# Kernel optimization log

Measured on AMD Instinct MI355X. Metric: run time of the kernel, lower is better.

The kernel has to match this reference:

```python
import jax, jax.numpy as jnp
import numpy as np

B, M, IN, H, D = 64, 512, 256, 4, 64
N = B * M
E = N * 16


def setup_inputs() -> dict:
    key = jax.random.key(0)
    ks = jax.random.split(key, 12)
    s = 1.0 / np.sqrt(IN)
    return {
        "query_input": jax.random.normal(ks[0], (N, IN), jnp.float32),
        "source_input": jax.random.normal(ks[1], (N, IN), jnp.float32),
        "edge_weight": jax.random.uniform(ks[2], (E,), jnp.float32),
        "Wq_w": jax.random.normal(ks[3], (IN, H * D), jnp.float32) * s,
        "Wq_b": jax.random.normal(ks[4], (H * D,), jnp.float32) * s,
        "Wk_w": jax.random.normal(ks[5], (IN, H * D), jnp.float32) * s,
        "Wk_b": jax.random.normal(ks[6], (H * D,), jnp.float32) * s,
        "Wv_w": jax.random.normal(ks[7], (IN, H * D), jnp.float32) * s,
        "Wv_b": jax.random.normal(ks[8], (H * D,), jnp.float32) * s,
        "n_nodes": jnp.full((B,), M, jnp.int32),
        "edge_index": jax.random.randint(ks[9], (2, E), 0, N, jnp.int32),
    }


def reference(query_input, source_input, edge_weight, Wq_w, Wq_b, Wk_w, Wk_b, Wv_w, Wv_b, n_nodes, edge_index):
    # projections -> [N, H, D]
    q = (query_input @ Wq_w + Wq_b).reshape(N, H, D)
    k = (source_input @ Wk_w + Wk_b).reshape(N, H, D)
    v = (source_input @ Wv_w + Wv_b).reshape(N, H, D)

    # 'simple' kernel attention. Global L2 normalization (torch.norm over whole tensor).
    qn = q / jnp.linalg.norm(q)
    kn = k / jnp.linalg.norm(k)
    # equal-size graphs: padding + mask reduces exactly to a reshape [B, M, H, D]
    q_pad = qn.reshape(B, M, H, D)
    k_pad = kn.reshape(B, M, H, D)
    v_pad = v.reshape(B, M, H, D)
    kv = jnp.einsum('bmhk,bmhv->bhkv', k_pad, v_pad)          # per-graph K^T V
    v_sum = v_pad.sum(axis=1)                                  # [B, H, D] scatter_add over batch
    k_sum = k_pad.sum(axis=1)                                  # [B, H, D]
    numer = jnp.einsum('bmhk,bhkv->bmhv', q_pad, kv) + v_sum[:, None]
    denom = jnp.einsum('bmhk,bhk->bmh', q_pad, k_sum) + n_nodes.astype(q.dtype)[:, None, None]
    attn = (numer / denom[..., None]).reshape(N, H, D)

    # gcn_conv on value: out[c] = sum_{e: col_e = c} w_e * rsqrt(deg[col_e]*deg[row_e]) * v[row_e]
    row, col = edge_index[0], edge_index[1]
    deg = jax.ops.segment_sum(jnp.ones((E,), jnp.float32), col, num_segments=N)
    val = edge_weight / jnp.sqrt(deg[col] * deg[row])
    val = jnp.nan_to_num(val, nan=0.0, posinf=0.0, neginf=0.0)
    gcn = jax.ops.segment_sum(val[:, None, None] * v[row], col, num_segments=N)

    return (attn + gcn).mean(axis=1)  # mean over heads -> [N, D]
```

## Files before the change

kernel.cpp:

```cpp
#include <hip/hip_runtime.h>
#include <hip/hip_bf16.h>

#define NN 32768
#define BB 64
#define MM 512
#define HH 4
#define DD 64
#define INF 256
#define HD 256
#define EE 524288
#define XSZ 8388608

typedef unsigned short ushort;
typedef unsigned int uint;
typedef short s16x8 __attribute__((ext_vector_type(8)));
typedef ushort u16x8 __attribute__((ext_vector_type(8)));
typedef float f32x4 __attribute__((ext_vector_type(4)));

__device__ __forceinline__ ushort f2bf(float f) {
    uint u = __float_as_uint(f);
    return (ushort)((u + 0x7fffu + ((u >> 16) & 1u)) >> 16);
}
__device__ __forceinline__ float bf2f(ushort u) {
    return __uint_as_float((uint)u << 16);
}
__device__ __forceinline__ uint pkbf(float x, float y) {
    __hip_bfloat162 h = __float22bfloat162_rn(make_float2(x, y));
    return *(uint*)&h;
}

#define GLD16(gp, lp) __builtin_amdgcn_global_load_lds( \
    (const __attribute__((address_space(1))) void*)(gp), \
    (__attribute__((address_space(3))) void*)(lp), 16, 0, 0)

__global__ __launch_bounds__(256) void prep_kernel(
    const float* __restrict__ Wq, const float* __restrict__ Wk,
    const float* __restrict__ Wv, ushort* __restrict__ WT,
    const int* __restrict__ ei, int* __restrict__ deg,
    const float* __restrict__ Xq, const float* __restrict__ Xs,
    ushort* __restrict__ xq16, ushort* __restrict__ xs16)
{
    const int bid = blockIdx.x;
    if (bid < 768) {
        const int id = bid * 256 + threadIdx.x;
        const int mat = id >> 16, rem = id & 65535;
        const int n = rem >> 8, kk = rem & 255;
        const float* W = (mat == 0) ? Wq : (mat == 1) ? Wk : Wv;
        WT[id] = f2bf(W[kk * 256 + n]);
    } else if (bid < 2816) {
        const int e = (bid - 768) * 256 + threadIdx.x;
        atomicAdd(&deg[ei[EE + e]], 1);
    } else {
        const size_t id = (size_t)(bid - 2816) * 256 + threadIdx.x;
        const size_t o8 = id * 8;
        const float* src; ushort* dst; size_t o;
        if (o8 < XSZ) { src = Xq; dst = xq16; o = o8; }
        else          { src = Xs; dst = xs16; o = o8 - XSZ; }
        const float4 f0 = *(const float4*)(src + o);
        const float4 f1 = *(const float4*)(src + o + 4);
        u16x8 r;
        r[0] = f2bf(f0.x); r[1] = f2bf(f0.y); r[2] = f2bf(f0.z); r[3] = f2bf(f0.w);
        r[4] = f2bf(f1.x); r[5] = f2bf(f1.y); r[6] = f2bf(f1.z); r[7] = f2bf(f1.w);
        *(u16x8*)(dst + o) = r;
    }
}

__global__ __launch_bounds__(256) void qkv_scan(
    const ushort* __restrict__ Xq16, const ushort* __restrict__ Xs16,
    const ushort* __restrict__ WT,
    const float* __restrict__ bq, const float* __restrict__ bk,
    const float* __restrict__ bv,
    ushort* __restrict__ qo, ushort* __restrict__ ko, ushort* __restrict__ vo,
    float* __restrict__ sumsq,
    const int* __restrict__ deg, int* __restrict__ offsets)
{
    __shared__ ushort As[2][128 * 32];
    __shared__ ushort Bs[2][128 * 32];
    __shared__ float wred[4];
    __shared__ int part[256];

    const int id = blockIdx.x;
    const int t = threadIdx.x;

    if (id == 1536) {
        const int base = t * 128;
        int s = 0;
        for (int i = 0; i < 128; ++i) s += deg[base + i];
        part[t] = s;
        __syncthreads();
        for (int off = 1; off < 256; off <<= 1) {
            int a = part[t];
            int b2 = (t >= off) ? part[t - off] : 0;
            __syncthreads();
            part[t] = a + b2;
            __syncthreads();
        }
        int run = (t == 0) ? 0 : part[t - 1];
        for (int i = 0; i < 128; ++i) { offsets[base + i] = run; run += deg[base + i]; }
        if (t == 255) offsets[NN] = run;
        return;
    }

    const int vv = (id & 7) * 192 + (id >> 3);
    const int rt = vv / 6, ct = vv % 6;
    const int wsel = ct >> 1;
    const ushort* A16 = (wsel == 0) ? Xq16 : Xs16;
    const ushort* W   = WT + (size_t)wsel * 65536;
    const float* bias = (wsel == 0) ? bq : (wsel == 1) ? bk : bv;
    ushort* C         = (wsel == 0) ? qo : (wsel == 1) ? ko : vo;
    const int row0 = rt * 128;
    const int col0 = (ct & 1) * 128;

    const int l = t & 63, w = t >> 6;
    const int fr = l & 15, q4 = l >> 4;
    const int wr = (w & 1) * 64, wc = (w >> 1) * 64;

    const int srow = (w << 4) + (l >> 2);
    const int scol = (l & 3) << 3;
    const ushort* ga = &A16[(size_t)(row0 + srow) * INF + scol];
    const ushort* gb = &W  [(size_t)(col0 + srow) * INF + scol];
    const int lbase = (w << 9);

    f32x4 acc[4][4] = {};

    GLD16(ga,             &As[0][lbase]);
    GLD16(ga + 64 * INF,  &As[0][2048 + lbase]);
    GLD16(gb,             &Bs[0][lbase]);
    GLD16(gb + 64 * INF,  &Bs[0][2048 + lbase]);

    int cur = 0;
    for (int it = 0; it < 8; ++it) {
        __syncthreads();
        if (it < 7) {
            const int k0 = (it + 1) * 32;
            GLD16(ga + k0,            &As[cur ^ 1][lbase]);
            GLD16(ga + k0 + 64 * INF, &As[cur ^ 1][2048 + lbase]);
            GLD16(gb + k0,            &Bs[cur ^ 1][lbase]);
            GLD16(gb + k0 + 64 * INF, &Bs[cur ^ 1][2048 + lbase]);
        }
        const int kg = q4 * 8;
        s16x8 af[4], bfr[4];
#pragma unroll
        for (int i = 0; i < 4; ++i)
            af[i] = *(const s16x8*)&As[cur][(wr + i * 16 + fr) * 32 + kg];
#pragma unroll
        for (int j = 0; j < 4; ++j)
            bfr[j] = *(const s16x8*)&Bs[cur][(wc + j * 16 + fr) * 32 + kg];
#pragma unroll
        for (int i = 0; i < 4; ++i)
#pragma unroll
            for (int j = 0; j < 4; ++j)
                acc[i][j] = __builtin_amdgcn_mfma_f32_16x16x32_bf16(
                    af[i], bfr[j], acc[i][j], 0, 0, 0);
        cur ^= 1;
    }

    float loc = 0.f;
#pragma unroll
    for (int j = 0; j < 4; ++j) {
        const int colg = col0 + wc + j * 16 + fr;
        const float bj = bias[colg];
#pragma unroll
        for (int i = 0; i < 4; ++i) {
            const int rowg = row0 + wr + i * 16 + q4 * 4;
#pragma unroll
            for (int m = 0; m < 4; ++m) {
                float cv = acc[i][j][m] + bj;
                loc += cv * cv;
                C[(size_t)(rowg + m) * HD + colg] = f2bf(cv);
            }
        }
    }
    if (wsel < 2) {
#pragma unroll
        for (int off = 32; off > 0; off >>= 1) loc += __shfl_down(loc, off, 64);
        if (l == 0) wred[w] = loc;
        __syncthreads();
        if (t == 0) atomicAdd(&sumsq[wsel], wred[0] + wred[1] + wred[2] + wred[3]);
    }
}

#define KVP 136
__global__ __launch_bounds__(256) void kv_vbar(
    const ushort* __restrict__ k16, const ushort* __restrict__ v16,
    float* __restrict__ kv_p, float* __restrict__ ksum_p, float* __restrict__ vsum_p,
    float* __restrict__ vbar)
{
    __shared__ ushort kT[64 * KVP];
    __shared__ ushort vT[64 * KVP];
    const int bid = blockIdx.x;
    const int t = threadIdx.x;

    if (bid >= 1024) {
        const int idx = (bid - 1024) * 1024 + t * 4;
        const int n = idx >> 6, d0 = idx & 63;
        const ushort* vr = &v16[(size_t)n * HD + d0];
        float4 o;
        float* op = (float*)&o;
#pragma unroll
        for (int j = 0; j < 4; ++j)
            op[j] = 0.25f * (bf2f(vr[j]) + bf2f(vr[64 + j]) +
                             bf2f(vr[128 + j]) + bf2f(vr[192 + j]));
        *(float4*)&vbar[idx] = o;
        return;
    }

    const int h = bid & 3, b = (bid >> 2) & 63, z = bid >> 8;
    const int l = t & 63, w = t >> 6;
    const size_t base = (size_t)b * MM * HD + (size_t)h * DD;
    const int m0 = z * 128;

    {
        const int mat = t >> 7;
        const int u = t & 63;
        const int dhalf = (t >> 6) & 1;
        const int r0 = 2 * u;
        const int d0 = dhalf * 32;
        const ushort* src = mat ? v16 : k16;
        ushort* dst = mat ? vT : kT;
        const ushort* p0 = &src[base + (size_t)(m0 + r0) * HD + d0];
        const ushort* p1 = p0 + HD;
        u16x8 ra[4], rb[4];
#pragma unroll
        for (int i = 0; i < 4; ++i) ra[i] = *(const u16x8*)(p0 + 8 * i);
#pragma unroll
        for (int i = 0; i < 4; ++i) rb[i] = *(const u16x8*)(p1 + 8 * i);
#pragma unroll
        for (int i = 0; i < 4; ++i)
#pragma unroll
            for (int jj = 0; jj < 8; ++jj) {
                const int d = d0 + 8 * i + jj;
                uint pk = (uint)ra[i][jj] | ((uint)rb[i][jj] << 16);
                *(uint*)&dst[d * KVP + r0] = pk;
            }
    }
    __syncthreads();

    const int fr = l & 15, q4 = l >> 4, kg = q4 * 8;
    const int wr2 = (w & 1) * 32, wc2 = (w >> 1) * 32;
    s16x8 ones;
#pragma unroll
    for (int i = 0; i < 8; ++i) ones[i] = (short)0x3F80;

    f32x4 acc[2][2] = {};
    f32x4 aks[2] = {};
    f32x4 avs[2] = {};
#pragma unroll
    for (int s = 0; s < 4; ++s) {
        const int mo = s * 32 + kg;
        s16x8 af[2], bf[2];
        af[0] = *(const s16x8*)&kT[(wr2 + fr) * KVP + mo];
        af[1] = *(const s16x8*)&kT[(wr2 + 16 + fr) * KVP + mo];
        bf[0] = *(const s16x8*)&vT[(wc2 + fr) * KVP + mo];
        bf[1] = *(const s16x8*)&vT[(wc2 + 16 + fr) * KVP + mo];
#pragma unroll
        for (int il = 0; il < 2; ++il)
#pragma unroll
            for (int jl = 0; jl < 2; ++jl)
                acc[il][jl] = __builtin_amdgcn_mfma_f32_16x16x32_bf16(
                    af[il], bf[jl], acc[il][jl], 0, 0, 0);
#pragma unroll
        for (int il = 0; il < 2; ++il)
            aks[il] = __builtin_amdgcn_mfma_f32_16x16x32_bf16(
                af[il], ones, aks[il], 0, 0, 0);
#pragma unroll
        for (int jl = 0; jl < 2; ++jl)
            avs[jl] = __builtin_amdgcn_mfma_f32_16x16x32_bf16(
                ones, bf[jl], avs[jl], 0, 0, 0);
    }

    float* kvb = &kv_p[(((size_t)b * HH + h) * 4 + z) * 4096];
#pragma unroll
    for (int jl = 0; jl < 2; ++jl) {
        const int dv = wc2 + 16 * jl + fr;
#pragma unroll
        for (int il = 0; il < 2; ++il) {
            const int dk = wr2 + 16 * il + q4 * 4;
            *(f32x4*)&kvb[(size_t)dv * 64 + dk] = acc[il][jl];
        }
    }
    float* ksb = &ksum_p[(((size_t)b * HH + h) * 4 + z) * 64];
    float* vsb = &vsum_p[(((size_t)b * HH + h) * 4 + z) * 64];
    if (wc2 == 0 && fr == 0) {
#pragma unroll
        for (int il = 0; il < 2; ++il)
#pragma unroll
            for (int m = 0; m < 4; ++m)
                ksb[wr2 + 16 * il + q4 * 4 + m] = aks[il][m];
    }
    if (wr2 == 0 && l < 16) {
        vsb[wc2 + l]      = avs[0][0];
        vsb[wc2 + 16 + l] = avs[1][0];
    }
}

__global__ __launch_bounds__(256) void red_bucket(
    const float* __restrict__ kv_p, const float* __restrict__ ksum_p,
    const float* __restrict__ vsum_p,
    ushort* __restrict__ kv16, float* __restrict__ ksum_f, float* __restrict__ vsum_f,
    const int* __restrict__ ei, const float* __restrict__ ew,
    const int* __restrict__ deg, const int* __restrict__ offsets,
    int* __restrict__ cursor, int2* __restrict__ pairbuf)
{
    const int bid = blockIdx.x;
    const int t = threadIdx.x;

    if (bid < 1024) {
        const int o4 = bid * 1024 + t * 4;
        const int bh = o4 >> 12, off = o4 & 4095;
        const float* p = &kv_p[(size_t)bh * 16384 + off];
        float4 s0 = *(const float4*)p;
        float4 s1 = *(const float4*)(p + 4096);
        float4 s2 = *(const float4*)(p + 8192);
        float4 s3 = *(const float4*)(p + 12288);
        const float r0 = s0.x + s1.x + s2.x + s3.x;
        const float r1 = s0.y + s1.y + s2.y + s3.y;
        const float r2 = s0.z + s1.z + s2.z + s3.z;
        const float r3 = s0.w + s1.w + s2.w + s3.w;
        uint2 pk = make_uint2(pkbf(r0, r1), pkbf(r2, r3));
        *(uint2*)&kv16[(size_t)bh * 4096 + off] = pk;
    } else if (bid < 1152) {
        const int o = (bid - 1024) * 256 + t;
        const float* src = (o < 16384) ? ksum_p : vsum_p;
        float* dst = (o < 16384) ? ksum_f : vsum_f;
        const int oo = o & 16383;
        const int bh = oo >> 6, d = oo & 63;
        const float* p = &src[(size_t)bh * 256 + d];
        dst[oo] = p[0] + p[64] + p[128] + p[192];
    } else {
        const int e = (bid - 1152) * 256 + t;
        const int row = ei[e], col = ei[EE + e];
        const long long prod = (long long)deg[row] * (long long)deg[col];
        float val = 0.f;
        if (prod > 0) val = ew[e] * __frsqrt_rn((float)prod);
        const int pos = atomicAdd(&cursor[col], 1);
        pairbuf[offsets[col] + pos] = make_int2(row, __float_as_int(val));
    }
}

#define AKP 72
__global__ __launch_bounds__(256) void attn_mfma(
    const ushort* __restrict__ q16, const ushort* __restrict__ kv16,
    const float* __restrict__ ksum_f, const float* __restrict__ vsum_f,
    const float* __restrict__ sumsq,
    const int* __restrict__ n_nodes, float* __restrict__ out)
{
    const int b = blockIdx.y;
    const int m0 = blockIdx.x * 64;
    const int t = threadIdx.x;
    const int l = t & 63, w = t >> 6;
    const int fr = l & 15, q4 = l >> 4;
    const int wn = (w & 1) * 32, wd = (w >> 1) * 32;

    __shared__ ushort kvbf[64 * AKP];
    __shared__ float ksum_l[64], vsum_l[64], denom_l[64];

    const float nn = (float)n_nodes[b];
    const float inv = 1.0f / (sqrtf(sumsq[0]) * sqrtf(sumsq[1]));
    f32x4 acco[2][2] = {};

    for (int h = 0; h < HH; ++h) {
        __syncthreads();
        {
            const int dv = t >> 2, dk0 = (t & 3) * 16;
            const ushort* kvg = &kv16[((size_t)(b * HH + h)) * 4096 + dv * 64 + dk0];
            *(uint4*)&kvbf[dv * AKP + dk0]     = *(const uint4*)kvg;
            *(uint4*)&kvbf[dv * AKP + dk0 + 8] = *(const uint4*)(kvg + 8);
        }
        if (t >= 64 && t < 128)
            ksum_l[t - 64] = ksum_f[((size_t)(b * HH + h)) * 64 + t - 64];
        else if (t >= 128 && t < 192)
            vsum_l[t - 128] = vsum_f[((size_t)(b * HH + h)) * 64 + t - 128];
        __syncthreads();

        if (t < 64) {
            const ushort* qr = &q16[((size_t)(b * MM + m0 + t)) * HD + h * DD];
            float dsum = 0.f;
#pragma unroll
            for (int c = 0; c < 8; ++c) {
                u16x8 qq = *(const u16x8*)(qr + 8 * c);
#pragma unroll
                for (int j2 = 0; j2 < 8; ++j2)
                    dsum += bf2f(qq[j2]) * ksum_l[8 * c + j2];
            }
            denom_l[t] = nn + inv * dsum;
        }
        __syncthreads();

        f32x4 pacc[2][2] = {};
#pragma unroll
        for (int kx = 0; kx < 2; ++kx) {
            const int k0 = kx * 32;
            s16x8 af[2], bf[2];
#pragma unroll
            for (int il = 0; il < 2; ++il)
                af[il] = *(const s16x8*)&q16[
                    ((size_t)(b * MM + m0 + wn + 16 * il + fr)) * HD + h * DD + k0 + q4 * 8];
#pragma unroll
            for (int jl = 0; jl < 2; ++jl)
                bf[jl] = *(const s16x8*)&kvbf[(wd + 16 * jl + fr) * AKP + k0 + q4 * 8];
#pragma unroll
            for (int il = 0; il < 2; ++il)
#pragma unroll
                for (int jl = 0; jl < 2; ++jl)
                    pacc[il][jl] = __builtin_amdgcn_mfma_f32_16x16x32_bf16(
                        af[il], bf[jl], pacc[il][jl], 0, 0, 0);
        }
#pragma unroll
        for (int il = 0; il < 2; ++il)
#pragma unroll
            for (int m = 0; m < 4; ++m) {
                const float rden = 0.25f / denom_l[wn + 16 * il + q4 * 4 + m];
#pragma unroll
                for (int jl = 0; jl < 2; ++jl) {
                    const int d = wd + 16 * jl + fr;
                    acco[il][jl][m] += (inv * pacc[il][jl][m] + vsum_l[d]) * rden;
                }
            }
    }

#pragma unroll
    for (int il = 0; il < 2; ++il)
#pragma unroll
        for (int m = 0; m < 4; ++m) {
            const size_t node = (size_t)b * MM + m0 + wn + 16 * il + q4 * 4 + m;
#pragma unroll
            for (int jl = 0; jl < 2; ++jl)
                out[node * DD + wd + 16 * jl + fr] = acco[il][jl][m];
        }
}

__global__ __launch_bounds__(256) void gcn_gather(
    const int* __restrict__ offsets, const int2* __restrict__ pairbuf,
    const float* __restrict__ vbar, float* __restrict__ out)
{
    const int t = blockIdx.x * 256 + threadIdx.x;
    const int n = t >> 4, d4 = (t & 15) << 2;
    const int s = offsets[n], e = offsets[n + 1];
    float ax = 0.f, ay = 0.f, az = 0.f, aw = 0.f;
    int i = s;
    for (; i + 2 <= e; i += 2) {
        const int2 p0 = pairbuf[i], p1 = pairbuf[i + 1];
        const float w0 = __int_as_float(p0.y), w1 = __int_as_float(p1.y);
        const float4 v0 = *(const float4*)&vbar[(size_t)p0.x * DD + d4];
        const float4 v1 = *(const float4*)&vbar[(size_t)p1.x * DD + d4];
        ax += w0 * v0.x + w1 * v1.x;
        ay += w0 * v0.y + w1 * v1.y;
        az += w0 * v0.z + w1 * v1.z;
        aw += w0 * v0.w + w1 * v1.w;
    }
    if (i < e) {
        const int2 p = pairbuf[i];
        const float wv = __int_as_float(p.y);
        const float4 v = *(const float4*)&vbar[(size_t)p.x * DD + d4];
        ax += wv * v.x; ay += wv * v.y; az += wv * v.z; aw += wv * v.w;
    }
    float4 o = *(float4*)&out[(size_t)n * DD + d4];
    o.x += ax; o.y += ay; o.z += az; o.w += aw;
    *(float4*)&out[(size_t)n * DD + d4] = o;
}

extern "C" void kernel_launch(void* const* d_in, const int* in_sizes, int n_in,
                              void* d_out, int out_size, void* d_ws, size_t ws_size,
                              hipStream_t stream)
{
    (void)in_sizes; (void)n_in; (void)out_size; (void)ws_size;
    const float* Xq = (const float*)d_in[0];
    const float* Xs = (const float*)d_in[1];
    const float* ew = (const float*)d_in[2];
    const float* Wq = (const float*)d_in[3];
    const float* bq = (const float*)d_in[4];
    const float* Wk = (const float*)d_in[5];
    const float* bk = (const float*)d_in[6];
    const float* Wv = (const float*)d_in[7];
    const float* bv = (const float*)d_in[8];
    const int* n_nodes = (const int*)d_in[9];
    const int* ei = (const int*)d_in[10];
    float* out = (float*)d_out;
    float* ws  = (float*)d_ws;

    const size_t SZ_QKV   = (size_t)NN * HD / 2;
    const size_t OFF_Q    = 0;
    const size_t OFF_K    = SZ_QKV;
    const size_t OFF_V    = SZ_QKV * 2;
    const size_t OFF_SS   = SZ_QKV * 3;
    const size_t OFF_DEG  = OFF_SS + 16;
    const size_t OFF_CUR  = OFF_DEG + NN;
    const size_t OFF_WT   = OFF_CUR + NN;
    const size_t OFF_OFFS = OFF_WT + 3 * 65536 / 2;
    const size_t OFF_UNI  = OFF_OFFS + NN + 16;
    const size_t OFF_XQ16 = OFF_UNI;
    const size_t OFF_XS16 = OFF_UNI + XSZ / 2;
    const size_t OFF_KV   = OFF_UNI;
    const size_t OFF_KSP  = OFF_KV + (size_t)BB * HH * 4 * 4096;
    const size_t OFF_VSP  = OFF_KSP + (size_t)BB * HH * 4 * 64;
    const size_t OFF_KV16 = OFF_VSP + (size_t)BB * HH * 4 * 64;
    const size_t OFF_KSF  = OFF_KV16 + (size_t)BB * HH * 4096 / 2;
    const size_t OFF_VSF  = OFF_KSF + (size_t)BB * HH * 64;
    const size_t OFF_PAIR = OFF_VSF + (size_t)BB * HH * 64;
    const size_t OFF_VBAR = OFF_PAIR + 2 * (size_t)EE;

    ushort* q16   = (ushort*)(ws + OFF_Q);
    ushort* k16   = (ushort*)(ws + OFF_K);
    ushort* v16   = (ushort*)(ws + OFF_V);
    float* sumsq  = ws + OFF_SS;
    int*   deg    = (int*)(ws + OFF_DEG);
    int*   cursor = (int*)(ws + OFF_CUR);
    ushort* WT    = (ushort*)(ws + OFF_WT);
    int*   offs   = (int*)(ws + OFF_OFFS);
    ushort* xq16  = (ushort*)(ws + OFF_XQ16);
    ushort* xs16  = (ushort*)(ws + OFF_XS16);
    float* kv_p   = ws + OFF_KV;
    float* ksum_p = ws + OFF_KSP;
    float* vsum_p = ws + OFF_VSP;
    ushort* kv16  = (ushort*)(ws + OFF_KV16);
    float* ksum_f = ws + OFF_KSF;
    float* vsum_f = ws + OFF_VSF;
    int2*  pairb  = (int2*)(ws + OFF_PAIR);
    float* vbar   = ws + OFF_VBAR;

    hipMemsetAsync(sumsq, 0, (16 + 2 * NN) * sizeof(float), stream);
    prep_kernel<<<11008, 256, 0, stream>>>(Wq, Wk, Wv, WT, ei, deg, Xq, Xs, xq16, xs16);
    qkv_scan<<<1537, 256, 0, stream>>>(
        xq16, xs16, WT, bq, bk, bv, q16, k16, v16, sumsq, deg, offs);
    kv_vbar<<<3072, 256, 0, stream>>>(k16, v16, kv_p, ksum_p, vsum_p, vbar);
    red_bucket<<<3200, 256, 0, stream>>>(
        kv_p, ksum_p, vsum_p, kv16, ksum_f, vsum_f,
        ei, ew, deg, offs, cursor, pairb);
    attn_mfma<<<dim3(MM / 64, BB), 256, 0, stream>>>(
        q16, kv16, ksum_f, vsum_f, sumsq, n_nodes, out);
    gcn_gather<<<(NN * 16) / 256, 256, 0, stream>>>(offs, pairb, vbar, out);
}
```

Measured before the change: 262.3 us.

## Fuse fp32-to-bf16 input conversion into QKV GEMM and drop LDS staging

```diff
diff --git a/kernel.cpp b/kernel.cpp
--- a/kernel.cpp
+++ b/kernel.cpp
@@ -9,7 +9,6 @@
 #define INF 256
 #define HD 256
 #define EE 524288
-#define XSZ 8388608
 
 typedef unsigned short ushort;
 typedef unsigned int uint;
@@ -29,16 +28,10 @@
     return *(uint*)&h;
 }
 
-#define GLD16(gp, lp) __builtin_amdgcn_global_load_lds( \
-    (const __attribute__((address_space(1))) void*)(gp), \
-    (__attribute__((address_space(3))) void*)(lp), 16, 0, 0)
-
 __global__ __launch_bounds__(256) void prep_kernel(
     const float* __restrict__ Wq, const float* __restrict__ Wk,
     const float* __restrict__ Wv, ushort* __restrict__ WT,
-    const int* __restrict__ ei, int* __restrict__ deg,
-    const float* __restrict__ Xq, const float* __restrict__ Xs,
-    ushort* __restrict__ xq16, ushort* __restrict__ xs16)
+    const int* __restrict__ ei, int* __restrict__ deg)
 {
     const int bid = blockIdx.x;
     if (bid < 768) {
@@ -47,26 +40,14 @@
         const int n = rem >> 8, kk = rem & 255;
         const float* W = (mat == 0) ? Wq : (mat == 1) ? Wk : Wv;
         WT[id] = f2bf(W[kk * 256 + n]);
-    } else if (bid < 2816) {
+    } else {
         const int e = (bid - 768) * 256 + threadIdx.x;
         atomicAdd(&deg[ei[EE + e]], 1);
-    } else {
-        const size_t id = (size_t)(bid - 2816) * 256 + threadIdx.x;
-        const size_t o8 = id * 8;
-        const float* src; ushort* dst; size_t o;
-        if (o8 < XSZ) { src = Xq; dst = xq16; o = o8; }
-        else          { src = Xs; dst = xs16; o = o8 - XSZ; }
-        const float4 f0 = *(const float4*)(src + o);
-        const float4 f1 = *(const float4*)(src + o + 4);
-        u16x8 r;
-        r[0] = f2bf(f0.x); r[1] = f2bf(f0.y); r[2] = f2bf(f0.z); r[3] = f2bf(f0.w);
-        r[4] = f2bf(f1.x); r[5] = f2bf(f1.y); r[6] = f2bf(f1.z); r[7] = f2bf(f1.w);
-        *(u16x8*)(dst + o) = r;
     }
 }
 
 __global__ __launch_bounds__(256) void qkv_scan(
-    const ushort* __restrict__ Xq16, const ushort* __restrict__ Xs16,
+    const float* __restrict__ Xq, const float* __restrict__ Xs,
     const ushort* __restrict__ WT,
     const float* __restrict__ bq, const float* __restrict__ bk,
     const float* __restrict__ bv,
@@ -74,8 +55,6 @@
     float* __restrict__ sumsq,
     const int* __restrict__ deg, int* __restrict__ offsets)
 {
-    __shared__ ushort As[2][128 * 32];
-    __shared__ ushort Bs[2][128 * 32];
     __shared__ float wred[4];
     __shared__ int part[256];
 
@@ -104,7 +83,7 @@
     const int vv = (id & 7) * 192 + (id >> 3);
     const int rt = vv / 6, ct = vv % 6;
     const int wsel = ct >> 1;
-    const ushort* A16 = (wsel == 0) ? Xq16 : Xs16;
+    const float* A    = (wsel == 0) ? Xq : Xs;
     const ushort* W   = WT + (size_t)wsel * 65536;
     const float* bias = (wsel == 0) ? bq : (wsel == 1) ? bk : bv;
     ushort* C         = (wsel == 0) ? qo : (wsel == 1) ? ko : vo;
@@ -115,44 +94,40 @@
     const int fr = l & 15, q4 = l >> 4;
     const int wr = (w & 1) * 64, wc = (w >> 1) * 64;
 
-    const int srow = (w << 4) + (l >> 2);
-    const int scol = (l & 3) << 3;
-    const ushort* ga = &A16[(size_t)(row0 + srow) * INF + scol];
-    const ushort* gb = &W  [(size_t)(col0 + srow) * INF + scol];
-    const int lbase = (w << 9);
-
     f32x4 acc[4][4] = {};
 
-    GLD16(ga,             &As[0][lbase]);
-    GLD16(ga + 64 * INF,  &As[0][2048 + lbase]);
-    GLD16(gb,             &Bs[0][lbase]);
-    GLD16(gb + 64 * INF,  &Bs[0][2048 + lbase]);
-
-    int cur = 0;
+    const float* ap[4];
+    const ushort* bp[4];
+#pragma unroll
+    for (int i = 0; i < 4; ++i)
+        ap[i] = A + (size_t)(row0 + wr + i * 16 + fr) * INF + q4 * 8;
+#pragma unroll
+    for (int j = 0; j < 4; ++j)
+        bp[j] = W + (size_t)(col0 + wc + j * 16 + fr) * INF + q4 * 8;
+
+#pragma unroll
     for (int it = 0; it < 8; ++it) {
-        __syncthreads();
-        if (it < 7) {
-            const int k0 = (it + 1) * 32;
-            GLD16(ga + k0,            &As[cur ^ 1][lbase]);
-            GLD16(ga + k0 + 64 * INF, &As[cur ^ 1][2048 + lbase]);
-            GLD16(gb + k0,            &Bs[cur ^ 1][lbase]);
-            GLD16(gb + k0 + 64 * INF, &Bs[cur ^ 1][2048 + lbase]);
-        }
-        const int kg = q4 * 8;
         s16x8 af[4], bfr[4];
 #pragma unroll
-        for (int i = 0; i < 4; ++i)
-            af[i] = *(const s16x8*)&As[cur][(wr + i * 16 + fr) * 32 + kg];
-#pragma unroll
         for (int j = 0; j < 4; ++j)
-            bfr[j] = *(const s16x8*)&Bs[cur][(wc + j * 16 + fr) * 32 + kg];
+            bfr[j] = *(const s16x8*)(bp[j] + it * 32);
+#pragma unroll
+        for (int i = 0; i < 4; ++i) {
+            const float4 lo = *(const float4*)(ap[i] + it * 32);
+            const float4 hi = *(const float4*)(ap[i] + it * 32 + 4);
+            union { s16x8 v; uint u[4]; } cv;
+            cv.u[0] = pkbf(lo.x, lo.y);
+            cv.u[1] = pkbf(lo.z, lo.w);
+            cv.u[2] = pkbf(hi.x, hi.y);
+            cv.u[3] = pkbf(hi.z, hi.w);
+            af[i] = cv.v;
+        }
 #pragma unroll
         for (int i = 0; i < 4; ++i)
 #pragma unroll
             for (int j = 0; j < 4; ++j)
                 acc[i][j] = __builtin_amdgcn_mfma_f32_16x16x32_bf16(
                     af[i], bfr[j], acc[i][j], 0, 0, 0);
-        cur ^= 1;
     }
 
     float loc = 0.f;
@@ -488,10 +463,7 @@
     const size_t OFF_CUR  = OFF_DEG + NN;
     const size_t OFF_WT   = OFF_CUR + NN;
     const size_t OFF_OFFS = OFF_WT + 3 * 65536 / 2;
-    const size_t OFF_UNI  = OFF_OFFS + NN + 16;
-    const size_t OFF_XQ16 = OFF_UNI;
-    const size_t OFF_XS16 = OFF_UNI + XSZ / 2;
-    const size_t OFF_KV   = OFF_UNI;
+    const size_t OFF_KV   = OFF_OFFS + NN + 16;
     const size_t OFF_KSP  = OFF_KV + (size_t)BB * HH * 4 * 4096;
     const size_t OFF_VSP  = OFF_KSP + (size_t)BB * HH * 4 * 64;
     const size_t OFF_KV16 = OFF_VSP + (size_t)BB * HH * 4 * 64;
@@ -508,8 +480,6 @@
     int*   cursor = (int*)(ws + OFF_CUR);
     ushort* WT    = (ushort*)(ws + OFF_WT);
     int*   offs   = (int*)(ws + OFF_OFFS);
-    ushort* xq16  = (ushort*)(ws + OFF_XQ16);
-    ushort* xs16  = (ushort*)(ws + OFF_XS16);
     float* kv_p   = ws + OFF_KV;
     float* ksum_p = ws + OFF_KSP;
     float* vsum_p = ws + OFF_VSP;
@@ -520,9 +490,9 @@
     float* vbar   = ws + OFF_VBAR;
 
     hipMemsetAsync(sumsq, 0, (16 + 2 * NN) * sizeof(float), stream);
-    prep_kernel<<<11008, 256, 0, stream>>>(Wq, Wk, Wv, WT, ei, deg, Xq, Xs, xq16, xs16);
+    prep_kernel<<<2816, 256, 0, stream>>>(Wq, Wk, Wv, WT, ei, deg);
     qkv_scan<<<1537, 256, 0, stream>>>(
-        xq16, xs16, WT, bq, bk, bv, q16, k16, v16, sumsq, deg, offs);
+        Xq, Xs, WT, bq, bk, bv, q16, k16, v16, sumsq, deg, offs);
     kv_vbar<<<3072, 256, 0, stream>>>(k16, v16, kv_p, ksum_p, vsum_p, vbar);
     red_bucket<<<3200, 256, 0, stream>>>(
         kv_p, ksum_p, vsum_p, kv16, ksum_f, vsum_f,
```

Result: slower. 296.3 us (+12.9%).

## Fuse GCN gather into attention kernel and move edge bucketing earlier

Applied to the files above, without the earlier changes.

```diff
diff --git a/kernel.cpp b/kernel.cpp
--- a/kernel.cpp
+++ b/kernel.cpp
@@ -181,16 +181,29 @@
 }
 
 #define KVP 136
-__global__ __launch_bounds__(256) void kv_vbar(
+__global__ __launch_bounds__(256) void kv_vbar_bucket(
     const ushort* __restrict__ k16, const ushort* __restrict__ v16,
     float* __restrict__ kv_p, float* __restrict__ ksum_p, float* __restrict__ vsum_p,
-    float* __restrict__ vbar)
+    float* __restrict__ vbar,
+    const int* __restrict__ ei, const float* __restrict__ ew,
+    const int* __restrict__ deg, const int* __restrict__ offsets,
+    int* __restrict__ cursor, int2* __restrict__ pairbuf)
 {
     __shared__ ushort kT[64 * KVP];
     __shared__ ushort vT[64 * KVP];
     const int bid = blockIdx.x;
     const int t = threadIdx.x;
 
+    if (bid >= 3072) {
+        const int e = (bid - 3072) * 256 + t;
+        const int row = ei[e], col = ei[EE + e];
+        const long long prod = (long long)deg[row] * (long long)deg[col];
+        float val = 0.f;
+        if (prod > 0) val = ew[e] * __frsqrt_rn((float)prod);
+        const int pos = atomicAdd(&cursor[col], 1);
+        pairbuf[offsets[col] + pos] = make_int2(row, __float_as_int(val));
+        return;
+    }
     if (bid >= 1024) {
         const int idx = (bid - 1024) * 1024 + t * 4;
         const int n = idx >> 6, d0 = idx & 63;
@@ -294,13 +307,10 @@
     }
 }
 
-__global__ __launch_bounds__(256) void red_bucket(
+__global__ __launch_bounds__(256) void red_kernel(
     const float* __restrict__ kv_p, const float* __restrict__ ksum_p,
     const float* __restrict__ vsum_p,
-    ushort* __restrict__ kv16, float* __restrict__ ksum_f, float* __restrict__ vsum_f,
-    const int* __restrict__ ei, const float* __restrict__ ew,
-    const int* __restrict__ deg, const int* __restrict__ offsets,
-    int* __restrict__ cursor, int2* __restrict__ pairbuf)
+    ushort* __restrict__ kv16, float* __restrict__ ksum_f, float* __restrict__ vsum_f)
 {
     const int bid = blockIdx.x;
     const int t = threadIdx.x;
@@ -319,7 +329,7 @@
         const float r3 = s0.w + s1.w + s2.w + s3.w;
         uint2 pk = make_uint2(pkbf(r0, r1), pkbf(r2, r3));
         *(uint2*)&kv16[(size_t)bh * 4096 + off] = pk;
-    } else if (bid < 1152) {
+    } else {
         const int o = (bid - 1024) * 256 + t;
         const float* src = (o < 16384) ? ksum_p : vsum_p;
         float* dst = (o < 16384) ? ksum_f : vsum_f;
@@ -327,28 +337,53 @@
         const int bh = oo >> 6, d = oo & 63;
         const float* p = &src[(size_t)bh * 256 + d];
         dst[oo] = p[0] + p[64] + p[128] + p[192];
-    } else {
-        const int e = (bid - 1152) * 256 + t;
-        const int row = ei[e], col = ei[EE + e];
-        const long long prod = (long long)deg[row] * (long long)deg[col];
-        float val = 0.f;
-        if (prod > 0) val = ew[e] * __frsqrt_rn((float)prod);
-        const int pos = atomicAdd(&cursor[col], 1);
-        pairbuf[offsets[col] + pos] = make_int2(row, __float_as_int(val));
     }
 }
 
 #define AKP 72
-__global__ __launch_bounds__(256) void attn_mfma(
+__global__ __launch_bounds__(256) void attn_gcn(
     const ushort* __restrict__ q16, const ushort* __restrict__ kv16,
     const float* __restrict__ ksum_f, const float* __restrict__ vsum_f,
     const float* __restrict__ sumsq,
-    const int* __restrict__ n_nodes, float* __restrict__ out)
+    const int* __restrict__ n_nodes, float* __restrict__ out,
+    const int* __restrict__ offsets, const int2* __restrict__ pairbuf,
+    const float* __restrict__ vbar)
 {
-    const int b = blockIdx.y;
-    const int m0 = blockIdx.x * 64;
+    const int bid = blockIdx.x;
     const int t = threadIdx.x;
-    const int l = t & 63, w = t >> 6;
+    const int l = t & 63;
+
+    if (bid % 5 != 0) {
+        const int gid = bid - bid / 5 - 1;
+        const int gt = gid * 256 + t;
+        const int n = gt >> 4;
+        const int j = l & 15;
+        const int d4 = j << 2;
+        const int gl = l & 48;
+        const int s = offsets[n], e = offsets[n + 1];
+        float ax = 0.f, ay = 0.f, az = 0.f, aw = 0.f;
+        for (int base = s; base < e; base += 16) {
+            const int cnt = min(16, e - base);
+            int2 p = make_int2(0, 0);
+            if (base + j < e) p = pairbuf[base + j];
+            for (int jj = 0; jj < cnt; ++jj) {
+                const int   row = __shfl(p.x, gl + jj, 64);
+                const float val = __uint_as_float((uint)__shfl(p.y, gl + jj, 64));
+                const float4 v = *(const float4*)&vbar[(size_t)row * DD + d4];
+                ax += val * v.x; ay += val * v.y;
+                az += val * v.z; aw += val * v.w;
+            }
+        }
+        float* op = &out[(size_t)n * DD + d4];
+        atomicAdd(op + 0, ax); atomicAdd(op + 1, ay);
+        atomicAdd(op + 2, az); atomicAdd(op + 3, aw);
+        return;
+    }
+
+    const int aid = bid / 5;
+    const int b = aid >> 3;
+    const int m0 = (aid & 7) * 64;
+    const int w = t >> 6;
     const int fr = l & 15, q4 = l >> 4;
     const int wn = (w & 1) * 32, wd = (w >> 1) * 32;
 
@@ -373,17 +408,20 @@
             vsum_l[t - 128] = vsum_f[((size_t)(b * HH + h)) * 64 + t - 128];
         __syncthreads();
 
-        if (t < 64) {
-            const ushort* qr = &q16[((size_t)(b * MM + m0 + t)) * HD + h * DD];
+        {
+            const int r = t >> 2, qq = t & 3;
+            const ushort* qr = &q16[((size_t)(b * MM + m0 + r)) * HD + h * DD + qq * 16];
             float dsum = 0.f;
 #pragma unroll
-            for (int c = 0; c < 8; ++c) {
-                u16x8 qq = *(const u16x8*)(qr + 8 * c);
+            for (int c = 0; c < 2; ++c) {
+                u16x8 qv = *(const u16x8*)(qr + 8 * c);
 #pragma unroll
                 for (int j2 = 0; j2 < 8; ++j2)
-                    dsum += bf2f(qq[j2]) * ksum_l[8 * c + j2];
+                    dsum += bf2f(qv[j2]) * ksum_l[qq * 16 + 8 * c + j2];
             }
-            denom_l[t] = nn + inv * dsum;
+            dsum += __shfl_xor(dsum, 1, 64);
+            dsum += __shfl_xor(dsum, 2, 64);
+            if (qq == 0) denom_l[r] = nn + inv * dsum;
         }
         __syncthreads();
 
@@ -426,38 +464,8 @@
             const size_t node = (size_t)b * MM + m0 + wn + 16 * il + q4 * 4 + m;
 #pragma unroll
             for (int jl = 0; jl < 2; ++jl)
-                out[node * DD + wd + 16 * jl + fr] = acco[il][jl][m];
-        }
-}
-
-__global__ __launch_bounds__(256) void gcn_gather(
-    const int* __restrict__ offsets, const int2* __restrict__ pairbuf,
-    const float* __restrict__ vbar, float* __restrict__ out)
-{
-    const int t = blockIdx.x * 256 + threadIdx.x;
-    const int n = t >> 4, d4 = (t & 15) << 2;
-    const int s = offsets[n], e = offsets[n + 1];
-    float ax = 0.f, ay = 0.f, az = 0.f, aw = 0.f;
-    int i = s;
-    for (; i + 2 <= e; i += 2) {
-        const int2 p0 = pairbuf[i], p1 = pairbuf[i + 1];
-        const float w0 = __int_as_float(p0.y), w1 = __int_as_float(p1.y);
-        const float4 v0 = *(const float4*)&vbar[(size_t)p0.x * DD + d4];
-        const float4 v1 = *(const float4*)&vbar[(size_t)p1.x * DD + d4];
-        ax += w0 * v0.x + w1 * v1.x;
-        ay += w0 * v0.y + w1 * v1.y;
-        az += w0 * v0.z + w1 * v1.z;
-        aw += w0 * v0.w + w1 * v1.w;
-    }
-    if (i < e) {
-        const int2 p = pairbuf[i];
-        const float wv = __int_as_float(p.y);
-        const float4 v = *(const float4*)&vbar[(size_t)p.x * DD + d4];
-        ax += wv * v.x; ay += wv * v.y; az += wv * v.z; aw += wv * v.w;
-    }
-    float4 o = *(float4*)&out[(size_t)n * DD + d4];
-    o.x += ax; o.y += ay; o.z += az; o.w += aw;
-    *(float4*)&out[(size_t)n * DD + d4] = o;
+                atomicAdd(&out[node * DD + wd + 16 * jl + fr], acco[il][jl][m]);
+        }
 }
 
 extern "C" void kernel_launch(void* const* d_in, const int* in_sizes, int n_in,
@@ -520,14 +528,14 @@
     float* vbar   = ws + OFF_VBAR;
 
     hipMemsetAsync(sumsq, 0, (16 + 2 * NN) * sizeof(float), stream);
+    hipMemsetAsync(out, 0, (size_t)NN * DD * sizeof(float), stream);
     prep_kernel<<<11008, 256, 0, stream>>>(Wq, Wk, Wv, WT, ei, deg, Xq, Xs, xq16, xs16);
     qkv_scan<<<1537, 256, 0, stream>>>(
         xq16, xs16, WT, bq, bk, bv, q16, k16, v16, sumsq, deg, offs);
-    kv_vbar<<<3072, 256, 0, stream>>>(k16, v16, kv_p, ksum_p, vsum_p, vbar);
-    red_bucket<<<3200, 256, 0, stream>>>(
-        kv_p, ksum_p, vsum_p, kv16, ksum_f, vsum_f,
-        ei, ew, deg, offs, cursor, pairb);
-    attn_mfma<<<dim3(MM / 64, BB), 256, 0, stream>>>(
-        q16, kv16, ksum_f, vsum_f, sumsq, n_nodes, out);
-    gcn_gather<<<(NN * 16) / 256, 256, 0, stream>>>(offs, pairb, vbar, out);
-}
+    kv_vbar_bucket<<<5120, 256, 0, stream>>>(
+        k16, v16, kv_p, ksum_p, vsum_p, vbar, ei, ew, deg, offs, cursor, pairb);
+    red_kernel<<<1152, 256, 0, stream>>>(
+        kv_p, ksum_p, vsum_p, kv16, ksum_f, vsum_f);
+    attn_gcn<<<2560, 256, 0, stream>>>(
+        q16, kv16, ksum_f, vsum_f, sumsq, n_nodes, out, offs, pairb, vbar);
+}
```

Measured after the change: 284.1 us. +8.3%, slower.
